# Optimization experiments

Hardware: AMD Instinct MI355X
Metric: run time of the kernel (lower is better)

Reference implementation:

```python
import jax, jax.numpy as jnp
import numpy as np

B, S, H = 2, 2048, 2048
NH, NKV, HD = 32, 8, 64
G = NH // NKV  # query heads per KV head
SCALE = HD ** -0.5
NEG = -1e9


def setup_inputs() -> dict:
    key = jax.random.key(0)
    ks = jax.random.split(key, 6)
    hidden_states = jax.random.normal(ks[0], (B, S, H), dtype=jnp.float32)
    # causal additive mask, broadcastable over batch and heads
    causal = jnp.tril(jnp.ones((S, S), dtype=bool))
    attention_mask = jnp.where(causal, 0.0, NEG).astype(jnp.float32)[None, None]
    sd = 1.0 / np.sqrt(H)
    wq = jax.random.normal(ks[1], (H, NH * HD), dtype=jnp.float32) * sd
    wk = jax.random.normal(ks[2], (H, NKV * HD), dtype=jnp.float32) * sd
    wv = jax.random.normal(ks[3], (H, NKV * HD), dtype=jnp.float32) * sd
    wo = jax.random.normal(ks[4], (NH * HD, H), dtype=jnp.float32) * sd
    return {"hidden_states": hidden_states, "attention_mask": attention_mask,
            "wq": wq, "wk": wk, "wv": wv, "wo": wo}


def reference(hidden_states, attention_mask, wq, wk, wv, wo):
    b, s, _ = hidden_states.shape
    # projections; group q heads as [b, kv_head, group, s, d] to avoid
    # materializing expanded K/V (same math as expand+matmul)
    q = (hidden_states @ wq).reshape(b, s, NKV, G, HD)
    k = (hidden_states @ wk).reshape(b, s, NKV, HD)
    v = (hidden_states @ wv).reshape(b, s, NKV, HD)
    q = jnp.einsum('bskgd->bkgsd', q)
    k = jnp.einsum('bskd->bksd', k)
    v = jnp.einsum('bskd->bksd', v)
    scores = jnp.einsum('bkgsd,bktd->bkgst', q, k) * SCALE  # [b,kv,G,s,s]
    mask = attention_mask  # [1,1,S,S] broadcastable
    scores = scores + mask[:, :, None] if mask.ndim == 4 else scores + mask
    attn = jax.nn.softmax(scores.astype(jnp.float32), axis=-1).astype(q.dtype)
    out = jnp.einsum('bkgst,bktd->bkgsd', attn, v)
    out = jnp.einsum('bkgsd->bskgd', out).reshape(b, s, NH * HD)
    return out @ wo
```

## Files before the change

kernel.cpp:

```cpp
#include <hip/hip_runtime.h>
#include <hip/hip_bf16.h>
#include <type_traits>


#define B_SZ 2
#define S_LEN 2048
#define HID 2048
#define NHEADS 32
#define NKVH 8
#define HEADD 64
#define QKV_N 3072
#define QK_SCALE 0.18033688f
#define FIXED_M 12.0f

typedef __attribute__((ext_vector_type(8))) short bf16x8;
typedef __attribute__((ext_vector_type(4))) float f32x4;

__device__ __forceinline__ float bf2f(unsigned short u) {
  union { unsigned int i; float f; } v;
  v.i = ((unsigned int)u) << 16;
  return v.f;
}
__device__ __forceinline__ unsigned short f2bf(float f) {
  union { float f; unsigned int i; } v;
  v.f = f;
  unsigned int r = v.i + 0x7fffu + ((v.i >> 16) & 1u);
  return (unsigned short)(r >> 16);
}
#if __has_builtin(__builtin_amdgcn_exp2f)
__device__ __forceinline__ float exp2v(float x) { return __builtin_amdgcn_exp2f(x); }
#else
__device__ __forceinline__ float exp2v(float x) { return exp2f(x); }
#endif
__device__ __forceinline__ void gload_lds16(const unsigned short* g, unsigned short* l) {
  __builtin_amdgcn_global_load_lds(
      (const __attribute__((address_space(1))) unsigned int*)g,
      (__attribute__((address_space(3))) unsigned int*)l, 16, 0, 0);
}
__device__ __forceinline__ int pv_perm(int s) {
  return (((s >> 2) & 7) << 3) | (((s >> 5) & 1) << 2) | (s & 3);
}

__global__ void cvt_bf16_kernel(const float4* __restrict__ in,
                                ushort4* __restrict__ out, int n4) {
  int i = blockIdx.x * blockDim.x + threadIdx.x;
  if (i >= n4) return;
  float4 v = in[i];
  ushort4 o;
  o.x = f2bf(v.x); o.y = f2bf(v.y); o.z = f2bf(v.z); o.w = f2bf(v.w);
  out[i] = o;
}

__global__ void transpose_qkvw_kernel(const float* __restrict__ wq,
                                      const float* __restrict__ wk,
                                      const float* __restrict__ wv,
                                      unsigned short* __restrict__ out) {
  __shared__ float tile[32][33];
  int n0 = blockIdx.x * 32;
  int r0 = blockIdx.y * 32;
  const float* src;
  int C, cb;
  float scale;
  if (n0 < 2048) { src = wq; C = 2048; cb = n0; scale = QK_SCALE; }
  else if (n0 < 2560) { src = wk; C = 512; cb = n0 - 2048; scale = 1.0f; }
  else { src = wv; C = 512; cb = n0 - 2560; scale = 1.0f; }
  int x = threadIdx.x, y = threadIdx.y;
#pragma unroll
  for (int i = 0; i < 32; i += 8)
    tile[y + i][x] = src[(size_t)(r0 + y + i) * C + cb + x];
  __syncthreads();
#pragma unroll
  for (int i = 0; i < 32; i += 8)
    out[(size_t)(n0 + y + i) * HID + r0 + x] = f2bf(tile[x][y + i] * scale);
}

__global__ void transpose_cvt_kernel(const float* __restrict__ in,
                                     unsigned short* __restrict__ out,
                                     int R, int C) {
  __shared__ float tile[32][33];
  int c0 = blockIdx.x * 32, r0 = blockIdx.y * 32;
  int x = threadIdx.x, y = threadIdx.y;
#pragma unroll
  for (int i = 0; i < 32; i += 8)
    tile[y + i][x] = in[(size_t)(r0 + y + i) * C + c0 + x];
  __syncthreads();
#pragma unroll
  for (int i = 0; i < 32; i += 8)
    out[(size_t)(c0 + y + i) * R + r0 + x] = f2bf(tile[x][y + i]);
}

__global__ void transpose_v_kernel(const unsigned short* __restrict__ QKV,
                                   unsigned short* __restrict__ Vt) {
  __shared__ unsigned short tile[32][33];
  int s0 = blockIdx.x * 32, d0 = blockIdx.y * 32;
  int bk = blockIdx.z;
  int b = bk >> 3, kvh = bk & 7;
  int x = threadIdx.x, y = threadIdx.y;
#pragma unroll
  for (int i = 0; i < 32; i += 8)
    tile[y + i][x] =
        QKV[(size_t)(b * S_LEN + s0 + y + i) * QKV_N + 2560 + kvh * HEADD + d0 + x];
  __syncthreads();
  int colg = s0 + x;
  int colp = (colg & ~63) | pv_perm(colg & 63);
#pragma unroll
  for (int i = 0; i < 32; i += 8)
    Vt[((size_t)(b * NKVH + kvh) * HEADD + d0 + y + i) * S_LEN + colp] =
        tile[x][y + i];
}

template <typename OutT>
__global__ __launch_bounds__(512, 2) void gemm256_kernel(
    const unsigned short* __restrict__ A, const unsigned short* __restrict__ Bt,
    OutT* __restrict__ C, int N, int K) {
  extern __shared__ unsigned short sm[];
  const int tid = threadIdx.x;
  const int wave = tid >> 6;
  const int lane = tid & 63;
  const int wm = wave >> 2, wn = wave & 3;
  const int rl = lane & 15, g = lane >> 4;
  const int nwg = gridDim.x;
  const int orig = blockIdx.x;
  const int swz = (orig & 7) * (nwg >> 3) + (orig >> 3);
  const int ntn = N >> 8;
  const int m0 = (swz / ntn) << 8;
  const int n0 = (swz % ntn) << 8;
  f32x4 acc[8][4] = {};

  size_t aoff[2], boff[2];
  int ldst[2];
#pragma unroll
  for (int i = 0; i < 2; ++i) {
    int cc = tid + i * 512;
    int row = cc >> 2, slot = cc & 3;
    int xk = (slot ^ ((row >> 1) & 3)) * 8;
    aoff[i] = (size_t)(m0 + row) * K + xk;
    boff[i] = (size_t)(n0 + row) * K + xk;
    ldst[i] = (wave * 64 + i * 512) * 8;
  }
  const int NT = K >> 6;

#pragma unroll
  for (int i = 0; i < 2; ++i) gload_lds16(A + aoff[i], sm + ldst[i]);
#pragma unroll
  for (int i = 0; i < 2; ++i) gload_lds16(Bt + boff[i], sm + 32768 + ldst[i]);
#pragma unroll
  for (int i = 0; i < 2; ++i) gload_lds16(A + aoff[i] + 32, sm + 8192 + ldst[i]);
#pragma unroll
  for (int i = 0; i < 2; ++i) gload_lds16(Bt + boff[i] + 32, sm + 40960 + ldst[i]);

  int cur = 0;
  for (int t = 0; t < NT; ++t) {
    const int nxt = cur ^ 1;
    const bool st = (t + 1 < NT);
    const size_t k1 = (size_t)(t + 1) << 6;
    unsigned short* An0 = sm + (nxt * 2 + 0) * 8192;
    unsigned short* An1 = sm + (nxt * 2 + 1) * 8192;
    unsigned short* Bn0 = sm + 32768 + (nxt * 2 + 0) * 8192;
    unsigned short* Bn1 = sm + 32768 + (nxt * 2 + 1) * 8192;
    const unsigned short* Ac0 = sm + (cur * 2 + 0) * 8192;
    const unsigned short* Ac1 = sm + (cur * 2 + 1) * 8192;
    const unsigned short* Bc0 = sm + 32768 + (cur * 2 + 0) * 8192;
    const unsigned short* Bc1 = sm + 32768 + (cur * 2 + 1) * 8192;
    bf16x8 bA[4], bB[4];
    if (st) {
      gload_lds16(A + aoff[0] + k1, An0 + ldst[0]);
      gload_lds16(A + aoff[1] + k1, An0 + ldst[1]);
    }
    __builtin_amdgcn_sched_barrier(0);
    if (st) asm volatile("s_waitcnt vmcnt(6)" ::: "memory");
    else    asm volatile("s_waitcnt vmcnt(4)" ::: "memory");
    __builtin_amdgcn_s_barrier();
    __builtin_amdgcn_sched_barrier(0);
#pragma unroll
    for (int nb = 0; nb < 4; ++nb) {
      int rw = wn * 64 + nb * 16 + rl;
      bB[nb] = *(const bf16x8*)&Bc0[rw * 32 + (g ^ ((rw >> 1) & 3)) * 8];
    }
#pragma unroll
    for (int mi = 0; mi < 4; ++mi) {
      int rw = wm * 128 + mi * 16 + rl;
      bA[mi] = *(const bf16x8*)&Ac0[rw * 32 + (g ^ ((rw >> 1) & 3)) * 8];
    }
    __builtin_amdgcn_s_setprio(1);
#pragma unroll
    for (int mi = 0; mi < 4; ++mi)
#pragma unroll
      for (int nb = 0; nb < 4; ++nb)
        acc[mi][nb] = __builtin_amdgcn_mfma_f32_16x16x32_bf16(bA[mi], bB[nb],
                                                              acc[mi][nb], 0, 0, 0);
    __builtin_amdgcn_s_setprio(0);
    if (st) {
      gload_lds16(Bt + boff[0] + k1, Bn0 + ldst[0]);
      gload_lds16(Bt + boff[1] + k1, Bn0 + ldst[1]);
    }
#pragma unroll
    for (int mi = 0; mi < 4; ++mi) {
      int rw = wm * 128 + 64 + mi * 16 + rl;
      bA[mi] = *(const bf16x8*)&Ac0[rw * 32 + (g ^ ((rw >> 1) & 3)) * 8];
    }
    __builtin_amdgcn_s_setprio(1);
#pragma unroll
    for (int mi = 0; mi < 4; ++mi)
#pragma unroll
      for (int nb = 0; nb < 4; ++nb)
        acc[4 + mi][nb] = __builtin_amdgcn_mfma_f32_16x16x32_bf16(bA[mi], bB[nb],
                                                                  acc[4 + mi][nb], 0, 0, 0);
    __builtin_amdgcn_s_setprio(0);
    if (st) {
      gload_lds16(A + aoff[0] + k1 + 32, An1 + ldst[0]);
      gload_lds16(A + aoff[1] + k1 + 32, An1 + ldst[1]);
    }
    __builtin_amdgcn_sched_barrier(0);
    if (st) asm volatile("s_waitcnt vmcnt(6)" ::: "memory");
    else    asm volatile("s_waitcnt vmcnt(0)" ::: "memory");
    __builtin_amdgcn_s_barrier();
    __builtin_amdgcn_sched_barrier(0);
#pragma unroll
    for (int nb = 0; nb < 4; ++nb) {
      int rw = wn * 64 + nb * 16 + rl;
      bB[nb] = *(const bf16x8*)&Bc1[rw * 32 + (g ^ ((rw >> 1) & 3)) * 8];
    }
#pragma unroll
    for (int mi = 0; mi < 4; ++mi) {
      int rw = wm * 128 + mi * 16 + rl;
      bA[mi] = *(const bf16x8*)&Ac1[rw * 32 + (g ^ ((rw >> 1) & 3)) * 8];
    }
    __builtin_amdgcn_s_setprio(1);
#pragma unroll
    for (int mi = 0; mi < 4; ++mi)
#pragma unroll
      for (int nb = 0; nb < 4; ++nb)
        acc[mi][nb] = __builtin_amdgcn_mfma_f32_16x16x32_bf16(bA[mi], bB[nb],
                                                              acc[mi][nb], 0, 0, 0);
    __builtin_amdgcn_s_setprio(0);
    if (st) {
      gload_lds16(Bt + boff[0] + k1 + 32, Bn1 + ldst[0]);
      gload_lds16(Bt + boff[1] + k1 + 32, Bn1 + ldst[1]);
    }
#pragma unroll
    for (int mi = 0; mi < 4; ++mi) {
      int rw = wm * 128 + 64 + mi * 16 + rl;
      bA[mi] = *(const bf16x8*)&Ac1[rw * 32 + (g ^ ((rw >> 1) & 3)) * 8];
    }
    __builtin_amdgcn_s_setprio(1);
#pragma unroll
    for (int mi = 0; mi < 4; ++mi)
#pragma unroll
      for (int nb = 0; nb < 4; ++nb)
        acc[4 + mi][nb] = __builtin_amdgcn_mfma_f32_16x16x32_bf16(bA[mi], bB[nb],
                                                                  acc[4 + mi][nb], 0, 0, 0);
    __builtin_amdgcn_s_setprio(0);
    cur = nxt;
  }
#pragma unroll
  for (int mg = 0; mg < 8; ++mg)
#pragma unroll
    for (int nb = 0; nb < 4; ++nb)
#pragma unroll
      for (int r = 0; r < 4; ++r) {
        int row = m0 + wm * 128 + (mg >> 2) * 64 + (mg & 3) * 16 + g * 4 + r;
        int col = n0 + wn * 64 + nb * 16 + rl;
        float v = acc[mg][nb][r];
        if constexpr (std::is_same_v<OutT, unsigned short>)
          C[(size_t)row * N + col] = f2bf(v);
        else
          C[(size_t)row * N + col] = v;
      }
}

__global__ __launch_bounds__(256) void mfma_attn_kernel(
    const unsigned short* __restrict__ QKV,
    const unsigned short* __restrict__ Vt,
    unsigned short* __restrict__ O) {
  __shared__ unsigned short Ks[2][64 * 64];
  __shared__ unsigned short Vs[2][64 * 64];
  const int head = blockIdx.y, b = blockIdx.z;
  const int kvh = head >> 2;
  const int tid = threadIdx.x;
  const int w = tid >> 6, lane = tid & 63;
  const int c = lane & 15, g = lane >> 4;
  const int srow = tid >> 3, sslot = tid & 7;
  const int xslot = sslot ^ (srow & 7);

  const unsigned short* Ksrc[2];
  const unsigned short* Vsrc[2];
#pragma unroll
  for (int i = 0; i < 2; ++i) {
    int row = srow + i * 32;
    Ksrc[i] = QKV + (size_t)(b * S_LEN + row) * QKV_N + 2048 + kvh * HEADD + xslot * 8;
    Vsrc[i] = Vt + ((size_t)(b * NKVH + kvh) * HEADD + row) * S_LEN + xslot * 8;
  }

#pragma unroll
  for (int i = 0; i < 2; ++i) {
    gload_lds16(Ksrc[i], &Ks[0][(w * 64 + i * 256) * 8]);
    gload_lds16(Vsrc[i], &Vs[0][(w * 64 + i * 256) * 8]);
  }
  __syncthreads();
  int cur = 0;

  for (int ph = 0; ph < 2; ++ph) {
    const int qt = (ph == 0) ? (int)blockIdx.x : (S_LEN / 64 - 1) - (int)blockIdx.x;
    bf16x8 qf[2];
    {
      const unsigned short* qp =
          QKV + (size_t)(b * S_LEN + qt * 64 + w * 16 + c) * QKV_N + head * HEADD +
          g * 8;
      qf[0] = *(const bf16x8*)(qp);
      qf[1] = *(const bf16x8*)(qp + 32);
    }
    f32x4 o_acc[4] = {};
    float lpart = 0.f;

    for (int t = 0; t <= qt; ++t) {
      const int kv0 = t * 64;
      const bool has_next = !(ph == 1 && t == qt);
      if (has_next) {
        const int kvn = (t < qt) ? kv0 + 64 : 0;
        const int nb = cur ^ 1;
#pragma unroll
        for (int i = 0; i < 2; ++i) {
          gload_lds16(Ksrc[i] + (size_t)kvn * QKV_N, &Ks[nb][(w * 64 + i * 256) * 8]);
          gload_lds16(Vsrc[i] + kvn, &Vs[nb][(w * 64 + i * 256) * 8]);
        }
      }
      f32x4 s_acc[4] = {};
      __builtin_amdgcn_s_setprio(1);
#pragma unroll
      for (int ks = 0; ks < 2; ++ks)
#pragma unroll
        for (int kn = 0; kn < 4; ++kn) {
          bf16x8 kf = *(const bf16x8*)&Ks[cur][(kn * 16 + c) * 64 +
                                              (((ks * 4 + g) ^ (c & 7)) * 8)];
          s_acc[kn] =
              __builtin_amdgcn_mfma_f32_16x16x32_bf16(kf, qf[ks], s_acc[kn], 0, 0, 0);
        }
      __builtin_amdgcn_s_setprio(0);
      if (t == qt) {
        const int qg = qt * 64 + w * 16 + c;
#pragma unroll
        for (int kn = 0; kn < 4; ++kn)
#pragma unroll
          for (int r = 0; r < 4; ++r)
            if (kv0 + kn * 16 + g * 4 + r > qg) s_acc[kn][r] = -1e30f;
      }
      float p[4][4];
#pragma unroll
      for (int kn = 0; kn < 4; ++kn)
#pragma unroll
        for (int r = 0; r < 4; ++r) {
          p[kn][r] = exp2v(s_acc[kn][r] - FIXED_M);
          lpart += p[kn][r];
        }
      union { bf16x8 v; unsigned int w4[4]; } afu[2];
#pragma unroll
      for (int b2 = 0; b2 < 2; ++b2) {
        afu[b2].w4[0] = __builtin_amdgcn_perm(__float_as_uint(p[b2][1]),
                                              __float_as_uint(p[b2][0]), 0x07060302u);
        afu[b2].w4[1] = __builtin_amdgcn_perm(__float_as_uint(p[b2][3]),
                                              __float_as_uint(p[b2][2]), 0x07060302u);
        afu[b2].w4[2] = __builtin_amdgcn_perm(__float_as_uint(p[2 + b2][1]),
                                              __float_as_uint(p[2 + b2][0]), 0x07060302u);
        afu[b2].w4[3] = __builtin_amdgcn_perm(__float_as_uint(p[2 + b2][3]),
                                              __float_as_uint(p[2 + b2][2]), 0x07060302u);
      }
      __builtin_amdgcn_s_setprio(1);
#pragma unroll
      for (int ks2 = 0; ks2 < 2; ++ks2)
#pragma unroll
        for (int dn = 0; dn < 4; ++dn) {
          bf16x8 vf = *(const bf16x8*)&Vs[cur][(dn * 16 + c) * 64 +
                                              (((ks2 * 4 + g) ^ (c & 7)) * 8)];
          o_acc[dn] =
              __builtin_amdgcn_mfma_f32_16x16x32_bf16(afu[ks2].v, vf, o_acc[dn], 0, 0, 0);
        }
      __builtin_amdgcn_s_setprio(0);
      __syncthreads();
      if (has_next) cur ^= 1;
    }
    float lsum = lpart;
    lsum += __shfl_xor(lsum, 16);
    lsum += __shfl_xor(lsum, 32);
    float inv = 1.0f / lsum;
    float invr[4];
#pragma unroll
    for (int r = 0; r < 4; ++r) invr[r] = __shfl(inv, g * 4 + r);
#pragma unroll
    for (int dn = 0; dn < 4; ++dn)
#pragma unroll
      for (int r = 0; r < 4; ++r) {
        int row = qt * 64 + w * 16 + g * 4 + r;
        int col = head * HEADD + dn * 16 + c;
        O[(size_t)(b * S_LEN + row) * (NHEADS * HEADD) + col] =
            f2bf(o_acc[dn][r] * invr[r]);
      }
  }
}

extern "C" void kernel_launch(void* const* d_in, const int* in_sizes, int n_in,
                              void* d_out, int out_size, void* d_ws, size_t ws_size,
                              hipStream_t stream) {
  const float* hs = (const float*)d_in[0];
  const float* wq = (const float*)d_in[2];
  const float* wk = (const float*)d_in[3];
  const float* wv = (const float*)d_in[4];
  const float* wo = (const float*)d_in[5];
  float* out = (float*)d_out;

  hipFuncSetAttribute(reinterpret_cast<const void*>(gemm256_kernel<unsigned short>),
                      hipFuncAttributeMaxDynamicSharedMemorySize, 131072);
  hipFuncSetAttribute(reinterpret_cast<const void*>(gemm256_kernel<float>),
                      hipFuncAttributeMaxDynamicSharedMemorySize, 131072);

  char* ws = (char*)d_ws;
  unsigned short* hs_bf = (unsigned short*)(ws);
  unsigned short* wAllT = (unsigned short*)(ws + ((size_t)16 << 20));
  unsigned short* woT  = (unsigned short*)(ws + ((size_t)28 << 20));
  unsigned short* QKV  = (unsigned short*)(ws + ((size_t)36 << 20));
  unsigned short* Ab   = (unsigned short*)(ws + ((size_t)60 << 20));
  unsigned short* VtB  = (unsigned short*)(ws + ((size_t)76 << 20));

  int n4 = (B_SZ * S_LEN * HID) / 4;
  cvt_bf16_kernel<<<n4 / 256, 256, 0, stream>>>((const float4*)hs, (ushort4*)hs_bf, n4);

  dim3 tb(32, 8);
  transpose_qkvw_kernel<<<dim3(96, 64), tb, 0, stream>>>(wq, wk, wv, wAllT);
  transpose_cvt_kernel<<<dim3(64, 64), tb, 0, stream>>>(wo, woT, NHEADS * HEADD, HID);

  gemm256_kernel<unsigned short><<<192, 512, 131072, stream>>>(
      hs_bf, wAllT, QKV, QKV_N, HID);

  transpose_v_kernel<<<dim3(S_LEN / 32, HEADD / 32, B_SZ * NKVH), tb, 0, stream>>>(
      QKV, VtB);

  mfma_attn_kernel<<<dim3(S_LEN / 128, NHEADS, B_SZ), 256, 0, stream>>>(QKV, VtB, Ab);

  gemm256_kernel<float><<<128, 512, 131072, stream>>>(
      Ab, woT, out, HID, HID);
}
```

Baseline: 195.7 us.

## Process 128-row query tiles per attention block with two 16-row subtiles per wave

Each wave now holds two 16-row query fragments, so the attention block covers 128 query rows, and each K/V tile loaded into LDS is reused across twice as many queries. The grid shrinks from 16 to 8 blocks along the query axis, still pairing a light and a heavy tile for causal balance. Per-subtile activity flags skip MFMAs for fully masked subtiles. The intent is to halve K/V LDS traffic and syncs per unit of work, at the cost of more registers, fewer blocks in flight, and more causal-diagonal waste.

```diff
diff --git a/kernel.cpp b/kernel.cpp
--- a/kernel.cpp
+++ b/kernel.cpp
@@ -301,23 +301,28 @@
   int cur = 0;
 
   for (int ph = 0; ph < 2; ++ph) {
-    const int qt = (ph == 0) ? (int)blockIdx.x : (S_LEN / 64 - 1) - (int)blockIdx.x;
-    bf16x8 qf[2];
+    const int qt = (ph == 0) ? (int)blockIdx.x : 15 - (int)blockIdx.x;
+    const int qg0 = qt * 128 + w * 32;
+    const int qg1 = qg0 + 16;
+    bf16x8 qf0[2], qf1[2];
     {
-      const unsigned short* qp =
-          QKV + (size_t)(b * S_LEN + qt * 64 + w * 16 + c) * QKV_N + head * HEADD +
-          g * 8;
-      qf[0] = *(const bf16x8*)(qp);
-      qf[1] = *(const bf16x8*)(qp + 32);
-    }
-    f32x4 o_acc[4] = {};
-    float lpart = 0.f;
-
-    for (int t = 0; t <= qt; ++t) {
+      const unsigned short* qp0 =
+          QKV + (size_t)(b * S_LEN + qg0 + c) * QKV_N + head * HEADD + g * 8;
+      qf0[0] = *(const bf16x8*)(qp0);
+      qf0[1] = *(const bf16x8*)(qp0 + 32);
+      const unsigned short* qp1 = qp0 + (size_t)16 * QKV_N;
+      qf1[0] = *(const bf16x8*)(qp1);
+      qf1[1] = *(const bf16x8*)(qp1 + 32);
+    }
+    f32x4 oa0[4] = {}, oa1[4] = {};
+    float lp0 = 0.f, lp1 = 0.f;
+
+    const int nt = 2 * qt + 2;
+    for (int t = 0; t < nt; ++t) {
       const int kv0 = t * 64;
-      const bool has_next = !(ph == 1 && t == qt);
+      const bool has_next = !(ph == 1 && t == nt - 1);
       if (has_next) {
-        const int kvn = (t < qt) ? kv0 + 64 : 0;
+        const int kvn = (t + 1 < nt) ? kv0 + 64 : 0;
         const int nb = cur ^ 1;
 #pragma unroll
         for (int i = 0; i < 2; ++i) {
@@ -325,76 +330,147 @@
           gload_lds16(Vsrc[i] + kvn, &Vs[nb][(w * 64 + i * 256) * 8]);
         }
       }
-      f32x4 s_acc[4] = {};
+      const bool act0 = (kv0 <= qg0 + 15);
+      const bool act1 = (kv0 <= qg1 + 15);
+      f32x4 sa0[4] = {}, sa1[4] = {};
       __builtin_amdgcn_s_setprio(1);
 #pragma unroll
-      for (int ks = 0; ks < 2; ++ks)
-#pragma unroll
-        for (int kn = 0; kn < 4; ++kn) {
-          bf16x8 kf = *(const bf16x8*)&Ks[cur][(kn * 16 + c) * 64 +
-                                              (((ks * 4 + g) ^ (c & 7)) * 8)];
-          s_acc[kn] =
-              __builtin_amdgcn_mfma_f32_16x16x32_bf16(kf, qf[ks], s_acc[kn], 0, 0, 0);
-        }
+      for (int ks = 0; ks < 2; ++ks) {
+        bf16x8 kf[4];
+#pragma unroll
+        for (int kn = 0; kn < 4; ++kn)
+          kf[kn] = *(const bf16x8*)&Ks[cur][(kn * 16 + c) * 64 +
+                                            (((ks * 4 + g) ^ (c & 7)) * 8)];
+        if (act0)
+#pragma unroll
+          for (int kn = 0; kn < 4; ++kn)
+            sa0[kn] = __builtin_amdgcn_mfma_f32_16x16x32_bf16(kf[kn], qf0[ks],
+                                                              sa0[kn], 0, 0, 0);
+        if (act1)
+#pragma unroll
+          for (int kn = 0; kn < 4; ++kn)
+            sa1[kn] = __builtin_amdgcn_mfma_f32_16x16x32_bf16(kf[kn], qf1[ks],
+                                                              sa1[kn], 0, 0, 0);
+      }
       __builtin_amdgcn_s_setprio(0);
-      if (t == qt) {
-        const int qg = qt * 64 + w * 16 + c;
+      union { bf16x8 v; unsigned int w4[4]; } af0[2], af1[2];
+      if (act0) {
+        if (kv0 + 63 > qg0) {
+          const int qrow = qg0 + c;
+#pragma unroll
+          for (int kn = 0; kn < 4; ++kn)
+#pragma unroll
+            for (int r = 0; r < 4; ++r)
+              if (kv0 + kn * 16 + g * 4 + r > qrow) sa0[kn][r] = -1e30f;
+        }
+        float p[4][4];
 #pragma unroll
         for (int kn = 0; kn < 4; ++kn)
 #pragma unroll
-          for (int r = 0; r < 4; ++r)
-            if (kv0 + kn * 16 + g * 4 + r > qg) s_acc[kn][r] = -1e30f;
+          for (int r = 0; r < 4; ++r) {
+            p[kn][r] = exp2v(sa0[kn][r] - FIXED_M);
+            lp0 += p[kn][r];
+          }
+#pragma unroll
+        for (int b2 = 0; b2 < 2; ++b2) {
+          af0[b2].w4[0] = __builtin_amdgcn_perm(__float_as_uint(p[b2][1]),
+                                                __float_as_uint(p[b2][0]), 0x07060302u);
+          af0[b2].w4[1] = __builtin_amdgcn_perm(__float_as_uint(p[b2][3]),
+                                                __float_as_uint(p[b2][2]), 0x07060302u);
+          af0[b2].w4[2] = __builtin_amdgcn_perm(__float_as_uint(p[2 + b2][1]),
+                                                __float_as_uint(p[2 + b2][0]), 0x07060302u);
+          af0[b2].w4[3] = __builtin_amdgcn_perm(__float_as_uint(p[2 + b2][3]),
+                                                __float_as_uint(p[2 + b2][2]), 0x07060302u);
+        }
       }
-      float p[4][4];
-#pragma unroll
-      for (int kn = 0; kn < 4; ++kn)
-#pragma unroll
-        for (int r = 0; r < 4; ++r) {
-          p[kn][r] = exp2v(s_acc[kn][r] - FIXED_M);
-          lpart += p[kn][r];
-        }
-      union { bf16x8 v; unsigned int w4[4]; } afu[2];
-#pragma unroll
-      for (int b2 = 0; b2 < 2; ++b2) {
-        afu[b2].w4[0] = __builtin_amdgcn_perm(__float_as_uint(p[b2][1]),
-                                              __float_as_uint(p[b2][0]), 0x07060302u);
-        afu[b2].w4[1] = __builtin_amdgcn_perm(__float_as_uint(p[b2][3]),
-                                              __float_as_uint(p[b2][2]), 0x07060302u);
-        afu[b2].w4[2] = __builtin_amdgcn_perm(__float_as_uint(p[2 + b2][1]),
-                                              __float_as_uint(p[2 + b2][0]), 0x07060302u);
-        afu[b2].w4[3] = __builtin_amdgcn_perm(__float_as_uint(p[2 + b2][3]),
-                                              __float_as_uint(p[2 + b2][2]), 0x07060302u);
+      if (act1) {
+        if (kv0 + 63 > qg1) {
+          const int qrow = qg1 + c;
+#pragma unroll
+          for (int kn = 0; kn < 4; ++kn)
+#pragma unroll
+            for (int r = 0; r < 4; ++r)
+              if (kv0 + kn * 16 + g * 4 + r > qrow) sa1[kn][r] = -1e30f;
+        }
+        float p[4][4];
+#pragma unroll
+        for (int kn = 0; kn < 4; ++kn)
+#pragma unroll
+          for (int r = 0; r < 4; ++r) {
+            p[kn][r] = exp2v(sa1[kn][r] - FIXED_M);
+            lp1 += p[kn][r];
+          }
+#pragma unroll
+        for (int b2 = 0; b2 < 2; ++b2) {
+          af1[b2].w4[0] = __builtin_amdgcn_perm(__float_as_uint(p[b2][1]),
+                                                __float_as_uint(p[b2][0]), 0x07060302u);
+          af1[b2].w4[1] = __builtin_amdgcn_perm(__float_as_uint(p[b2][3]),
+                                                __float_as_uint(p[b2][2]), 0x07060302u);
+          af1[b2].w4[2] = __builtin_amdgcn_perm(__float_as_uint(p[2 + b2][1]),
+                                                __float_as_uint(p[2 + b2][0]), 0x07060302u);
+          af1[b2].w4[3] = __builtin_amdgcn_perm(__float_as_uint(p[2 + b2][3]),
+                                                __float_as_uint(p[2 + b2][2]), 0x07060302u);
+        }
       }
       __builtin_amdgcn_s_setprio(1);
 #pragma unroll
-      for (int ks2 = 0; ks2 < 2; ++ks2)
-#pragma unroll
-        for (int dn = 0; dn < 4; ++dn) {
-          bf16x8 vf = *(const bf16x8*)&Vs[cur][(dn * 16 + c) * 64 +
-                                              (((ks2 * 4 + g) ^ (c & 7)) * 8)];
-          o_acc[dn] =
-              __builtin_amdgcn_mfma_f32_16x16x32_bf16(afu[ks2].v, vf, o_acc[dn], 0, 0, 0);
-        }
+      for (int ks2 = 0; ks2 < 2; ++ks2) {
+        bf16x8 vf[4];
+#pragma unroll
+        for (int dn = 0; dn < 4; ++dn)
+          vf[dn] = *(const bf16x8*)&Vs[cur][(dn * 16 + c) * 64 +
+                                            (((ks2 * 4 + g) ^ (c & 7)) * 8)];
+        if (act0)
+#pragma unroll
+          for (int dn = 0; dn < 4; ++dn)
+            oa0[dn] = __builtin_amdgcn_mfma_f32_16x16x32_bf16(af0[ks2].v, vf[dn],
+                                                              oa0[dn], 0, 0, 0);
+        if (act1)
+#pragma unroll
+          for (int dn = 0; dn < 4; ++dn)
+            oa1[dn] = __builtin_amdgcn_mfma_f32_16x16x32_bf16(af1[ks2].v, vf[dn],
+                                                              oa1[dn], 0, 0, 0);
+      }
       __builtin_amdgcn_s_setprio(0);
       __syncthreads();
       if (has_next) cur ^= 1;
     }
-    float lsum = lpart;
-    lsum += __shfl_xor(lsum, 16);
-    lsum += __shfl_xor(lsum, 32);
-    float inv = 1.0f / lsum;
-    float invr[4];
-#pragma unroll
-    for (int r = 0; r < 4; ++r) invr[r] = __shfl(inv, g * 4 + r);
-#pragma unroll
-    for (int dn = 0; dn < 4; ++dn)
-#pragma unroll
-      for (int r = 0; r < 4; ++r) {
-        int row = qt * 64 + w * 16 + g * 4 + r;
-        int col = head * HEADD + dn * 16 + c;
-        O[(size_t)(b * S_LEN + row) * (NHEADS * HEADD) + col] =
-            f2bf(o_acc[dn][r] * invr[r]);
-      }
+    {
+      float lsum = lp0;
+      lsum += __shfl_xor(lsum, 16);
+      lsum += __shfl_xor(lsum, 32);
+      float inv = 1.0f / lsum;
+      float invr[4];
+#pragma unroll
+      for (int r = 0; r < 4; ++r) invr[r] = __shfl(inv, g * 4 + r);
+#pragma unroll
+      for (int dn = 0; dn < 4; ++dn)
+#pragma unroll
+        for (int r = 0; r < 4; ++r) {
+          int row = qg0 + g * 4 + r;
+          int col = head * HEADD + dn * 16 + c;
+          O[(size_t)(b * S_LEN + row) * (NHEADS * HEADD) + col] =
+              f2bf(oa0[dn][r] * invr[r]);
+        }
+    }
+    {
+      float lsum = lp1;
+      lsum += __shfl_xor(lsum, 16);
+      lsum += __shfl_xor(lsum, 32);
+      float inv = 1.0f / lsum;
+      float invr[4];
+#pragma unroll
+      for (int r = 0; r < 4; ++r) invr[r] = __shfl(inv, g * 4 + r);
+#pragma unroll
+      for (int dn = 0; dn < 4; ++dn)
+#pragma unroll
+        for (int r = 0; r < 4; ++r) {
+          int row = qg1 + g * 4 + r;
+          int col = head * HEADD + dn * 16 + c;
+          O[(size_t)(b * S_LEN + row) * (NHEADS * HEADD) + col] =
+              f2bf(oa1[dn][r] * invr[r]);
+        }
+    }
   }
 }
 
@@ -434,7 +510,7 @@
   transpose_v_kernel<<<dim3(S_LEN / 32, HEADD / 32, B_SZ * NKVH), tb, 0, stream>>>(
       QKV, VtB);
 
-  mfma_attn_kernel<<<dim3(S_LEN / 128, NHEADS, B_SZ), 256, 0, stream>>>(QKV, VtB, Ab);
+  mfma_attn_kernel<<<dim3(8, NHEADS, B_SZ), 256, 0, stream>>>(QKV, VtB, Ab);
 
   gemm256_kernel<float><<<128, 512, 131072, stream>>>(
       Ab, woT, out, HID, HID);
```

After: 213.1 us. 8.9% more time.

## Use 128x128 tiled GEMM for output projection and MFMA-based softmax row sums

Applied to the files above, without the earlier changes.

Replaces the 256-tile GEMM for the output projection (which launched only 128 blocks) with a new 128x128-tile, 3-stage LDS-pipelined GEMM launched on 512 blocks. The aim is better CU occupancy and load balance on a 4096x2048x2048 problem. Separately, the attention kernel now computes softmax denominators with an extra MFMA against a vector of ones instead of scalar adds and cross-lane shuffles. This adds MFMA work but removes VALU adds and shuffles, and the sum is now accumulated from bf16-rounded probabilities.

```diff
diff --git a/kernel.cpp b/kernel.cpp
--- a/kernel.cpp
+++ b/kernel.cpp
@@ -269,6 +269,96 @@
       }
 }
 
+template <typename OutT>
+__global__ __launch_bounds__(256) void gemm_bt_kernel(
+    const unsigned short* __restrict__ A, const unsigned short* __restrict__ Bt,
+    OutT* __restrict__ C, int M, int N, int K) {
+  __shared__ unsigned short ldsA[3][128 * 32];
+  __shared__ unsigned short ldsB[3][128 * 32];
+  const int tid = threadIdx.x;
+  const int wave = tid >> 6;
+  const int lane = tid & 63;
+  const int nwg = gridDim.x;
+  const int orig = blockIdx.x;
+  const int swz = (orig & 7) * (nwg >> 3) + (orig >> 3);
+  const int ntn = N >> 7;
+  const int m0 = (swz / ntn) << 7;
+  const int n0 = (swz % ntn) << 7;
+  const int wr = wave >> 1, wc = wave & 1;
+  f32x4 acc[4][4] = {};
+
+  size_t offA[2], offB[2];
+#pragma unroll
+  for (int i = 0; i < 2; ++i) {
+    int cc = tid + i * 256;
+    int row = cc >> 2, slot = cc & 3;
+    int xk = (slot ^ ((row >> 1) & 3)) * 8;
+    offA[i] = (size_t)(m0 + row) * K + xk;
+    offB[i] = (size_t)(n0 + row) * K + xk;
+  }
+  const int rl = lane & 15, g = lane >> 4;
+  const int nk = K >> 5;
+  const int ldsbase = (wave * 64) * 8;
+
+#pragma unroll
+  for (int s = 0; s < 2; ++s) {
+#pragma unroll
+    for (int i = 0; i < 2; ++i) {
+      gload_lds16(A + offA[i] + (s << 5), &ldsA[s][ldsbase + i * 256 * 8]);
+      gload_lds16(Bt + offB[i] + (s << 5), &ldsB[s][ldsbase + i * 256 * 8]);
+    }
+  }
+  int cur = 0;
+
+  for (int t = 0; t < nk; ++t) {
+    __builtin_amdgcn_sched_barrier(0);
+    if (t < nk - 1)
+      asm volatile("s_waitcnt vmcnt(4)" ::: "memory");
+    else
+      asm volatile("s_waitcnt vmcnt(0)" ::: "memory");
+    __builtin_amdgcn_s_barrier();
+    __builtin_amdgcn_sched_barrier(0);
+    if (t + 2 < nk) {
+      const int k0 = (t + 2) << 5;
+      const int nb = (cur + 2 >= 3) ? cur - 1 : cur + 2;
+#pragma unroll
+      for (int i = 0; i < 2; ++i) {
+        gload_lds16(A + offA[i] + k0, &ldsA[nb][ldsbase + i * 256 * 8]);
+        gload_lds16(Bt + offB[i] + k0, &ldsB[nb][ldsbase + i * 256 * 8]);
+      }
+    }
+    const int xs = (g ^ ((rl >> 1) & 3)) * 8;
+    bf16x8 a[4], b[4];
+#pragma unroll
+    for (int mi = 0; mi < 4; ++mi)
+      a[mi] = *(const bf16x8*)&ldsA[cur][(wr * 64 + mi * 16 + rl) * 32 + xs];
+#pragma unroll
+    for (int ni = 0; ni < 4; ++ni)
+      b[ni] = *(const bf16x8*)&ldsB[cur][(wc * 64 + ni * 16 + rl) * 32 + xs];
+#pragma unroll
+    for (int mi = 0; mi < 4; ++mi)
+#pragma unroll
+      for (int ni = 0; ni < 4; ++ni)
+        acc[mi][ni] =
+            __builtin_amdgcn_mfma_f32_16x16x32_bf16(a[mi], b[ni], acc[mi][ni], 0, 0, 0);
+    cur = (cur + 1 == 3) ? 0 : cur + 1;
+  }
+#pragma unroll
+  for (int mi = 0; mi < 4; ++mi)
+#pragma unroll
+    for (int ni = 0; ni < 4; ++ni)
+#pragma unroll
+      for (int r = 0; r < 4; ++r) {
+        int row = m0 + wr * 64 + mi * 16 + (lane >> 4) * 4 + r;
+        int col = n0 + wc * 64 + ni * 16 + (lane & 15);
+        float v = acc[mi][ni][r];
+        if constexpr (std::is_same_v<OutT, unsigned short>)
+          C[(size_t)row * N + col] = f2bf(v);
+        else
+          C[(size_t)row * N + col] = v;
+      }
+}
+
 __global__ __launch_bounds__(256) void mfma_attn_kernel(
     const unsigned short* __restrict__ QKV,
     const unsigned short* __restrict__ Vt,
@@ -283,6 +373,10 @@
   const int srow = tid >> 3, sslot = tid & 7;
   const int xslot = sslot ^ (srow & 7);
 
+  bf16x8 ones_f;
+#pragma unroll
+  for (int i = 0; i < 8; ++i) ones_f[i] = (short)0x3F80;
+
   const unsigned short* Ksrc[2];
   const unsigned short* Vsrc[2];
 #pragma unroll
@@ -311,7 +405,7 @@
       qf[1] = *(const bf16x8*)(qp + 32);
     }
     f32x4 o_acc[4] = {};
-    float lpart = 0.f;
+    f32x4 l_acc = {};
 
     for (int t = 0; t <= qt; ++t) {
       const int kv0 = t * 64;
@@ -349,10 +443,8 @@
 #pragma unroll
       for (int kn = 0; kn < 4; ++kn)
 #pragma unroll
-        for (int r = 0; r < 4; ++r) {
+        for (int r = 0; r < 4; ++r)
           p[kn][r] = exp2v(s_acc[kn][r] - FIXED_M);
-          lpart += p[kn][r];
-        }
       union { bf16x8 v; unsigned int w4[4]; } afu[2];
 #pragma unroll
       for (int b2 = 0; b2 < 2; ++b2) {
@@ -367,7 +459,7 @@
       }
       __builtin_amdgcn_s_setprio(1);
 #pragma unroll
-      for (int ks2 = 0; ks2 < 2; ++ks2)
+      for (int ks2 = 0; ks2 < 2; ++ks2) {
 #pragma unroll
         for (int dn = 0; dn < 4; ++dn) {
           bf16x8 vf = *(const bf16x8*)&Vs[cur][(dn * 16 + c) * 64 +
@@ -375,26 +467,23 @@
           o_acc[dn] =
               __builtin_amdgcn_mfma_f32_16x16x32_bf16(afu[ks2].v, vf, o_acc[dn], 0, 0, 0);
         }
+        l_acc = __builtin_amdgcn_mfma_f32_16x16x32_bf16(afu[ks2].v, ones_f, l_acc, 0, 0, 0);
+      }
       __builtin_amdgcn_s_setprio(0);
       __syncthreads();
       if (has_next) cur ^= 1;
     }
-    float lsum = lpart;
-    lsum += __shfl_xor(lsum, 16);
-    lsum += __shfl_xor(lsum, 32);
-    float inv = 1.0f / lsum;
-    float invr[4];
-#pragma unroll
-    for (int r = 0; r < 4; ++r) invr[r] = __shfl(inv, g * 4 + r);
-#pragma unroll
-    for (int dn = 0; dn < 4; ++dn)
-#pragma unroll
-      for (int r = 0; r < 4; ++r) {
-        int row = qt * 64 + w * 16 + g * 4 + r;
+#pragma unroll
+    for (int r = 0; r < 4; ++r) {
+      float inv = 1.0f / l_acc[r];
+      int row = qt * 64 + w * 16 + g * 4 + r;
+#pragma unroll
+      for (int dn = 0; dn < 4; ++dn) {
         int col = head * HEADD + dn * 16 + c;
         O[(size_t)(b * S_LEN + row) * (NHEADS * HEADD) + col] =
-            f2bf(o_acc[dn][r] * invr[r]);
-      }
+            f2bf(o_acc[dn][r] * inv);
+      }
+    }
   }
 }
 
@@ -410,8 +499,6 @@
 
   hipFuncSetAttribute(reinterpret_cast<const void*>(gemm256_kernel<unsigned short>),
                       hipFuncAttributeMaxDynamicSharedMemorySize, 131072);
-  hipFuncSetAttribute(reinterpret_cast<const void*>(gemm256_kernel<float>),
-                      hipFuncAttributeMaxDynamicSharedMemorySize, 131072);
 
   char* ws = (char*)d_ws;
   unsigned short* hs_bf = (unsigned short*)(ws);
@@ -436,6 +523,6 @@
 
   mfma_attn_kernel<<<dim3(S_LEN / 128, NHEADS, B_SZ), 256, 0, stream>>>(QKV, VtB, Ab);
 
-  gemm256_kernel<float><<<128, 512, 131072, stream>>>(
-      Ab, woT, out, HID, HID);
-}
+  gemm_bt_kernel<float><<<32 * 16, 256, 0, stream>>>(
+      Ab, woT, out, B_SZ * S_LEN, HID, HID);
+}
```

Measured after the change: 190.0 us. 2.9% less time.
